# Performance work log

Hardware: AMD Instinct MI355X
Metric: run time of the kernel (lower is better)

The kernel has to match this reference:

```python
import jax, jax.numpy as jnp
import numpy as np

B, LQ, LK, D, H, DK = 128, 32, 128, 1024, 16, 64


def setup_inputs() -> dict:
    key = jax.random.key(0)
    ks = jax.random.split(key, 10)
    Q_seq = jax.random.normal(ks[0], (B, LQ, D), dtype=jnp.float32)
    K_seq = jax.random.normal(ks[1], (B, LK, D), dtype=jnp.float32)
    V_seq = jax.random.normal(ks[2], (B, LK, D), dtype=jnp.float32)
    title_mask = (jax.random.uniform(ks[3], (B, LQ)) < 0.9).astype(jnp.float32)
    body_mask = (jax.random.uniform(ks[4], (B, LQ, LK)) < 0.9).astype(jnp.float32)
    s = 1.0 / np.sqrt(D)
    Wq = jax.random.uniform(ks[5], (H * DK, D), jnp.float32, -s, s)
    Wk = jax.random.uniform(ks[6], (H * DK, D), jnp.float32, -s, s)
    Wv = jax.random.uniform(ks[7], (H * DK, D), jnp.float32, -s, s)
    bq = jnp.zeros((H * DK,), jnp.float32)
    bk = jnp.zeros((H * DK,), jnp.float32)
    bv = jnp.zeros((H * DK,), jnp.float32)
    return {"Q_seq": Q_seq, "K_seq": K_seq, "V_seq": V_seq,
            "title_mask": title_mask, "body_mask": body_mask,
            "Wq": Wq, "bq": bq, "Wk": Wk, "bk": bk, "Wv": Wv, "bv": bv}


def reference(Q_seq, K_seq, V_seq, title_mask, body_mask, Wq, bq, Wk, bk, Wv, bv):
    b = Q_seq.shape[0]
    # concatenate title tokens onto keys/values: [B, LK+LQ, D]
    K_cat = jnp.concatenate([K_seq, Q_seq], axis=1)
    V_cat = jnp.concatenate([V_seq, Q_seq], axis=1)
    # mask: [B, LQ, LK+LQ]
    tmask_rep = jnp.broadcast_to(title_mask[:, None, :], (b, LQ, LQ))
    mask = jnp.concatenate([body_mask, tmask_rep], axis=2) * title_mask[:, :, None]
    # projections -> [B, H, len, DK]
    Qh = (Q_seq @ Wq.T + bq).reshape(b, LQ, H, DK).transpose(0, 2, 1, 3)
    Kh = (K_cat @ Wk.T + bk).reshape(b, LK + LQ, H, DK).transpose(0, 2, 1, 3)
    Vh = (V_cat @ Wv.T + bv).reshape(b, LK + LQ, H, DK).transpose(0, 2, 1, 3)
    # custom exp-based masked attention (non-softmax normalization)
    scores = jnp.einsum('bhqd,bhkd->bhqk', Qh, Kh) / np.sqrt(float(DK))
    scores = jnp.exp(scores) * mask[:, None, :, :]
    attn = scores / (jnp.sum(scores, axis=-1, keepdims=True) + 1e-8)
    ctx = jnp.einsum('bhqk,bhkd->bhqd', attn, Vh)
    return ctx.transpose(0, 2, 1, 3).reshape(b, LQ, H * DK)
```

## Files before the change

### kernel.cpp

```cpp
#include <hip/hip_runtime.h>

typedef _Float16 f16;
typedef _Float16 f16x2 __attribute__((ext_vector_type(2)));
typedef _Float16 f16x4 __attribute__((ext_vector_type(4)));
typedef _Float16 f16x8 __attribute__((ext_vector_type(8)));
typedef float f32x4v __attribute__((ext_vector_type(4)));

#define AS1 __attribute__((address_space(1)))
#define AS3 __attribute__((address_space(3)))

__device__ __forceinline__ void gload_lds16(const f16* g, f16* l) {
  __builtin_amdgcn_global_load_lds((const AS1 unsigned int*)g,
                                   (AS3 unsigned int*)l, 16, 0, 0);
}

__global__ __launch_bounds__(256) void prep_kernel(
    const float* __restrict__ Q_seq, const float* __restrict__ K_seq,
    const float* __restrict__ V_seq,
    const float* __restrict__ Wq, const float* __restrict__ Wk,
    const float* __restrict__ Wv,
    f16* __restrict__ Qb, f16* __restrict__ Kb, f16* __restrict__ Vb,
    f16* __restrict__ Wqb, f16* __restrict__ Wkb, f16* __restrict__ Wvb)
{
  const long long g = (long long)blockIdx.x * 256 + threadIdx.x;
  const float* s;
  f16* d;
  if (g < 524288) {
    s = Q_seq + g * 8; d = Qb + g * 8;
  } else if (g < 2621440) {
    long long e = (g - 524288) * 8; s = K_seq + e; d = Kb + e;
  } else if (g < 4718592) {
    long long e = (g - 2621440) * 8; s = V_seq + e; d = Vb + e;
  } else if (g < 4849664) {
    long long e = (g - 4718592) * 8; s = Wq + e; d = Wqb + e;
  } else if (g < 4980736) {
    long long e = (g - 4849664) * 8; s = Wk + e; d = Wkb + e;
  } else {
    long long e = (g - 4980736) * 8; s = Wv + e; d = Wvb + e;
  }
  float4 v0 = *(const float4*)s;
  float4 v1 = *(const float4*)(s + 4);
  f16x8 o;
  o[0] = (f16)v0.x; o[1] = (f16)v0.y; o[2] = (f16)v0.z; o[3] = (f16)v0.w;
  o[4] = (f16)v1.x; o[5] = (f16)v1.y; o[6] = (f16)v1.z; o[7] = (f16)v1.w;
  *(f16x8*)d = o;
}

__device__ __forceinline__ void gemm_tile_128(
    const f16* __restrict__ A, const f16* __restrict__ W,
    const float* __restrict__ bias, f16* __restrict__ C,
    int m0, int n0, int rowShift, int outStride, int rowOff,
    f16* sbuf)
{
  f16* As0 = sbuf;
  f16* Bs0 = sbuf + 8192;

  const int t = threadIdx.x;
  const int w = t >> 6, lane = t & 63;
  const int wr = w >> 1, wc = w & 1;
  const int sr = lane >> 2, sc = (lane & 3) * 8;

  const f16* gA0 = A + (long long)(m0 + w * 32 + sr) * 1024 + sc;
  const f16* gA1 = A + (long long)(m0 + w * 32 + 16 + sr) * 1024 + sc;
  const f16* gB0 = W + (long long)(n0 + w * 32 + sr) * 1024 + sc;
  const f16* gB1 = W + (long long)(n0 + w * 32 + 16 + sr) * 1024 + sc;
  f16* lA0 = As0 + (w * 32) * 32;
  f16* lA1 = As0 + (w * 32 + 16) * 32;
  f16* lB0 = Bs0 + (w * 32) * 32;
  f16* lB1 = Bs0 + (w * 32 + 16) * 32;

  f32x4v acc[4][4];
#pragma unroll
  for (int i = 0; i < 4; ++i)
#pragma unroll
    for (int j = 0; j < 4; ++j) acc[i][j] = (f32x4v){0.f, 0.f, 0.f, 0.f};

  const int fr = lane & 15;
  const int fk = (lane >> 4) * 8;
  const f16* pA = As0 + (wr * 64 + fr) * 32 + fk;
  const f16* pB = Bs0 + (wc * 64 + fr) * 32 + fk;

  for (int k0 = 0; k0 < 1024; k0 += 64) {
    gload_lds16(gA0 + k0, lA0);
    gload_lds16(gA1 + k0, lA1);
    gload_lds16(gA0 + k0 + 32, lA0 + 4096);
    gload_lds16(gA1 + k0 + 32, lA1 + 4096);
    gload_lds16(gB0 + k0, lB0);
    gload_lds16(gB1 + k0, lB1);
    gload_lds16(gB0 + k0 + 32, lB0 + 4096);
    gload_lds16(gB1 + k0 + 32, lB1 + 4096);
    __syncthreads();
#pragma unroll
    for (int kk = 0; kk < 2; ++kk) {
      f16x8 av[4], bv[4];
#pragma unroll
      for (int i = 0; i < 4; ++i)
        av[i] = *(const f16x8*)(pA + kk * 4096 + i * 16 * 32);
#pragma unroll
      for (int i = 0; i < 4; ++i)
        bv[i] = *(const f16x8*)(pB + kk * 4096 + i * 16 * 32);
#pragma unroll
      for (int i = 0; i < 4; ++i)
#pragma unroll
        for (int j = 0; j < 4; ++j)
          acc[i][j] = __builtin_amdgcn_mfma_f32_16x16x32_f16(av[i], bv[j],
                                                             acc[i][j], 0, 0, 0);
    }
    __syncthreads();
  }

  f16* Cs = sbuf;
  float bn[4];
#pragma unroll
  for (int j = 0; j < 4; ++j) bn[j] = bias[n0 + wc * 64 + j * 16 + fr];
  const int g4 = (lane >> 4) * 4;
#pragma unroll
  for (int i = 0; i < 4; ++i) {
#pragma unroll
    for (int j = 0; j < 4; ++j) {
#pragma unroll
      for (int v = 0; v < 4; ++v) {
        int row = wr * 64 + i * 16 + g4 + v;
        int col = wc * 64 + j * 16 + fr;
        Cs[row * 136 + (col ^ ((row & 12) << 2))] = (f16)(acc[i][j][v] + bn[j]);
      }
    }
  }
  __syncthreads();

  const int rowMask = (1 << rowShift) - 1;
  const int row = t >> 1, half = t & 1;
  const int rsw = (row & 12) << 2;
  const int arow = m0 + row;
  const int orow = (arow >> rowShift) * outStride + (arow & rowMask) + rowOff;
  f16* dst = C + (long long)orow * 1024 + n0 + half * 64;
  const f16* srcr = Cs + row * 136;
#pragma unroll
  for (int c = 0; c < 8; ++c)
    *(f16x8*)(dst + c * 8) = *(const f16x8*)(srcr + ((half * 64 + c * 8) ^ rsw));
}

__global__ __launch_bounds__(256) void gemm_kv2(
    const f16* __restrict__ Kb, const f16* __restrict__ Wkb,
    const float* __restrict__ bk, f16* __restrict__ Kh,
    const f16* __restrict__ Vb, const f16* __restrict__ Wvb,
    const float* __restrict__ bv, f16* __restrict__ Vh)
{
  __shared__ __align__(16) f16 sbuf[128 * 136];
  const int bid = blockIdx.x;
  const int v = (bid & 7) * 256 + (bid >> 3);
  const int z = v >> 10, rem = v & 1023;
  const int by = rem >> 3, bx = rem & 7;
  const f16* A = z ? Vb : Kb;
  const f16* W = z ? Wvb : Wkb;
  const float* bias = z ? bv : bk;
  f16* C = z ? Vh : Kh;
  gemm_tile_128(A, W, bias, C, by * 128, bx * 128, 7, 160, 0, sbuf);
}

__global__ __launch_bounds__(256) void gemm_q3(
    const f16* __restrict__ Qb,
    const f16* __restrict__ Wqb, const f16* __restrict__ Wkb,
    const f16* __restrict__ Wvb,
    const float* __restrict__ bq, const float* __restrict__ bk,
    const float* __restrict__ bv,
    f16* __restrict__ Qh, f16* __restrict__ Kh, f16* __restrict__ Vh)
{
  __shared__ __align__(16) f16 sbuf[128 * 136];
  const int bid = blockIdx.x;
  const int v = (bid & 7) * 96 + (bid >> 3);
  const int z = v >> 8, rem = v & 255;
  const int by = rem >> 3, bx = rem & 7;
  const f16* W = (z == 0) ? Wqb : (z == 1) ? Wkb : Wvb;
  const float* bias = (z == 0) ? bq : (z == 1) ? bk : bv;
  f16* C = (z == 0) ? Qh : (z == 1) ? Kh : Vh;
  const int outStride = (z == 0) ? 32 : 160;
  const int rowOff = (z == 0) ? 0 : 128;
  gemm_tile_128(Qb, W, bias, C, by * 128, bx * 128, 5, outStride, rowOff, sbuf);
}

__global__ __launch_bounds__(256) void attn_kernel(
    const f16* __restrict__ Qh, const f16* __restrict__ Kh,
    const f16* __restrict__ Vh,
    const float* __restrict__ title, const float* __restrict__ body,
    float* __restrict__ out)
{
  __shared__ __align__(16) f16 Qs[32 * 72];
  __shared__ __align__(16) f16 Ks[160 * 72];
  __shared__ __align__(16) f16 Vs[160 * 68];
  __shared__ float rs[4][32];
  __shared__ float invs[32];

  const int bh = blockIdx.x, b = bh >> 4, h = bh & 15;
  const int t = threadIdx.x, w = t >> 6, lane = t & 63;
  const int c = lane & 15, g = lane >> 4;

  const long long qbase = ((long long)(b * 32) << 10) + h * 64;
  const long long kbase = ((long long)(b * 160) << 10) + h * 64;

  {
    int row = t >> 3, ch = t & 7;
    *(f16x8*)(Qs + row * 72 + ch * 8) =
        *(const f16x8*)(Qh + qbase + (long long)row * 1024 + ch * 8);
  }
#pragma unroll
  for (int r = 0; r < 5; ++r) {
    int i = t + r * 256;
    int row = i >> 3, ch = i & 7;
    *(f16x8*)(Ks + row * 72 + ch * 8) =
        *(const f16x8*)(Kh + kbase + (long long)row * 1024 + ch * 8);
    f16x8 vv = *(const f16x8*)(Vh + kbase + (long long)row * 1024 + ch * 8);
    f16x4 vlo = __builtin_shufflevector(vv, vv, 0, 1, 2, 3);
    f16x4 vhi = __builtin_shufflevector(vv, vv, 4, 5, 6, 7);
    *(f16x4*)(Vs + row * 68 + ch * 8) = vlo;
    *(f16x4*)(Vs + row * 68 + ch * 8 + 4) = vhi;
  }
  __syncthreads();

  f16x8 qf[2][2];
#pragma unroll
  for (int qt = 0; qt < 2; ++qt)
#pragma unroll
    for (int s = 0; s < 2; ++s)
      qf[qt][s] = *(const f16x8*)(Qs + (qt * 16 + c) * 72 + s * 32 + g * 8);

  const int cnt = (w < 2) ? 3 : 2;
  const int tile0 = (w < 2) ? w * 3 : 6 + (w - 2) * 2;

  f16x4 pp[3][2];
  float rsum[2] = {0.f, 0.f};

#pragma unroll
  for (int i = 0; i < 3; ++i) {
    if (i < cnt) {
      const int kt = tile0 + i;
      f16x8 kf0 = *(const f16x8*)(Ks + (kt * 16 + c) * 72 + 0 + g * 8);
      f16x8 kf1 = *(const f16x8*)(Ks + (kt * 16 + c) * 72 + 32 + g * 8);
#pragma unroll
      for (int qt = 0; qt < 2; ++qt) {
        f32x4v s4 = (f32x4v){0.f, 0.f, 0.f, 0.f};
        s4 = __builtin_amdgcn_mfma_f32_16x16x32_f16(kf0, qf[qt][0], s4, 0, 0, 0);
        s4 = __builtin_amdgcn_mfma_f32_16x16x32_f16(kf1, qf[qt][1], s4, 0, 0, 0);
        float4 m4;
        if (kt < 8) {
          m4 = *(const float4*)(body +
                ((long long)(b * 32 + qt * 16 + c)) * 128 + kt * 16 + 4 * g);
        } else {
          m4 = *(const float4*)(title + b * 32 + (kt - 8) * 16 + 4 * g);
        }
        float e0 = __expf(s4[0] * 0.125f) * m4.x;
        float e1 = __expf(s4[1] * 0.125f) * m4.y;
        float e2 = __expf(s4[2] * 0.125f) * m4.z;
        float e3 = __expf(s4[3] * 0.125f) * m4.w;
        rsum[qt] += (e0 + e1) + (e2 + e3);
        f16x4 p4;
        p4.x = (f16)e0; p4.y = (f16)e1; p4.z = (f16)e2; p4.w = (f16)e3;
        pp[i][qt] = p4;
      }
    }
  }

#pragma unroll
  for (int qt = 0; qt < 2; ++qt) {
    rsum[qt] += __shfl_xor(rsum[qt], 16);
    rsum[qt] += __shfl_xor(rsum[qt], 32);
  }
  if (lane < 16) {
    rs[w][c] = rsum[0];
    rs[w][16 + c] = rsum[1];
  }
  __syncthreads();

  f16* Ps = Ks;
#pragma unroll
  for (int i = 0; i < 3; ++i) {
    if (i < cnt) {
      const int kt = tile0 + i;
#pragma unroll
      for (int qt = 0; qt < 2; ++qt)
        *(f16x4*)(Ps + (qt * 16 + c) * 168 + kt * 16 + 4 * g) = pp[i][qt];
    }
  }
  if (t < 32) {
    float ssum = rs[0][t] + rs[1][t] + rs[2][t] + rs[3][t];
    invs[t] = title[b * 32 + t] / (ssum + 1e-8f);
  }
  __syncthreads();

  f32x4v o[2] = {(f32x4v){0.f, 0.f, 0.f, 0.f}, (f32x4v){0.f, 0.f, 0.f, 0.f}};
#pragma unroll
  for (int s = 0; s < 5; ++s) {
    f16x8 vf;
#pragma unroll
    for (int j = 0; j < 8; ++j)
      vf[j] = Vs[(32 * s + 8 * g + j) * 68 + 16 * w + c];
#pragma unroll
    for (int qt = 0; qt < 2; ++qt) {
      f16x8 pf = *(const f16x8*)(Ps + (qt * 16 + c) * 168 + s * 32 + g * 8);
      o[qt] = __builtin_amdgcn_mfma_f32_16x16x32_f16(pf, vf, o[qt], 0, 0, 0);
    }
  }

#pragma unroll
  for (int qt = 0; qt < 2; ++qt) {
#pragma unroll
    for (int v = 0; v < 4; ++v) {
      int q = qt * 16 + 4 * g + v;
      out[((long long)(b * 32 + q) << 10) + h * 64 + 16 * w + c] =
          o[qt][v] * invs[q];
    }
  }
}

extern "C" void kernel_launch(void* const* d_in, const int* in_sizes, int n_in,
                              void* d_out, int out_size, void* d_ws, size_t ws_size,
                              hipStream_t stream) {
  const float* Q_seq = (const float*)d_in[0];
  const float* K_seq = (const float*)d_in[1];
  const float* V_seq = (const float*)d_in[2];
  const float* title = (const float*)d_in[3];
  const float* body  = (const float*)d_in[4];
  const float* Wq = (const float*)d_in[5];
  const float* bq = (const float*)d_in[6];
  const float* Wk = (const float*)d_in[7];
  const float* bk = (const float*)d_in[8];
  const float* Wv = (const float*)d_in[9];
  const float* bv = (const float*)d_in[10];
  float* out = (float*)d_out;

  f16* ws = (f16*)d_ws;
  f16* Qb  = ws;
  f16* Kb  = Qb + 4194304;
  f16* Vb  = Kb + 16777216;
  f16* Wqb = Vb + 16777216;
  f16* Wkb = Wqb + 1048576;
  f16* Wvb = Wkb + 1048576;
  f16* Qh  = Wvb + 1048576;
  f16* Kh  = Qh + 4194304;
  f16* Vh  = Kh + 20971520;

  prep_kernel<<<19968, 256, 0, stream>>>(Q_seq, K_seq, V_seq, Wq, Wk, Wv,
                                         Qb, Kb, Vb, Wqb, Wkb, Wvb);
  gemm_kv2<<<2048, 256, 0, stream>>>(Kb, Wkb, bk, Kh, Vb, Wvb, bv, Vh);
  gemm_q3<<<768, 256, 0, stream>>>(Qb, Wqb, Wkb, Wvb, bq, bk, bv,
                                   Qh, Kh, Vh);
  attn_kernel<<<2048, 256, 0, stream>>>(Qh, Kh, Vh, title, body, out);
}
```

Baseline: 208.6 us.

## Enlarge projection GEMM tiles to 256x256 with double-buffered LDS pipeline

Replaces the 128x128 single-buffered GEMM tile with a 256x256 tile computed by 512 threads. The LDS buffers are double-buffered, with global_load_lds prefetch two K-tiles ahead, an XOR swizzle on the LDS layout, explicit waitcnt and barrier scheduling, and setprio around the MFMA bursts. The larger tile is meant to raise operand reuse and hide global-load latency behind MFMA work. In exchange it uses 128KB of LDS and occupancy of 1 block per CU, and gemm_q3 now launches only 192 blocks, which may underfill the GPU.

```diff
diff --git a/kernel.cpp b/kernel.cpp
--- a/kernel.cpp
+++ b/kernel.cpp
@@ -46,83 +46,119 @@
   *(f16x8*)d = o;
 }
 
-__device__ __forceinline__ void gemm_tile_128(
+__device__ __forceinline__ void gemm_tile_256(
     const f16* __restrict__ A, const f16* __restrict__ W,
     const float* __restrict__ bias, f16* __restrict__ C,
     int m0, int n0, int rowShift, int outStride, int rowOff,
     f16* sbuf)
 {
-  f16* As0 = sbuf;
-  f16* Bs0 = sbuf + 8192;
-
   const int t = threadIdx.x;
   const int w = t >> 6, lane = t & 63;
-  const int wr = w >> 1, wc = w & 1;
-  const int sr = lane >> 2, sc = (lane & 3) * 8;
-
-  const f16* gA0 = A + (long long)(m0 + w * 32 + sr) * 1024 + sc;
-  const f16* gA1 = A + (long long)(m0 + w * 32 + 16 + sr) * 1024 + sc;
-  const f16* gB0 = W + (long long)(n0 + w * 32 + sr) * 1024 + sc;
-  const f16* gB1 = W + (long long)(n0 + w * 32 + 16 + sr) * 1024 + sc;
-  f16* lA0 = As0 + (w * 32) * 32;
-  f16* lA1 = As0 + (w * 32 + 16) * 32;
-  f16* lB0 = Bs0 + (w * 32) * 32;
-  f16* lB1 = Bs0 + (w * 32 + 16) * 32;
-
-  f32x4v acc[4][4];
-#pragma unroll
-  for (int i = 0; i < 4; ++i)
+  const int wr = w >> 2, wc = w & 3;
+  const int fr = lane & 15, g = lane >> 4;
+  const int lrow = lane >> 3;
+  const int kgr = (lane & 7) ^ lrow;
+
+  const f16* aSrc[4];
+  const f16* bSrc[4];
+#pragma unroll
+  for (int s = 0; s < 4; ++s) {
+    aSrc[s] = A + (long long)(m0 + (w * 4 + s) * 8 + lrow) * 1024 + kgr * 8;
+    bSrc[s] = W + (long long)(n0 + (w * 4 + s) * 8 + lrow) * 1024 + kgr * 8;
+  }
+
+#define STAGE(tile)                                                          \
+  {                                                                          \
+    f16* ab_ = sbuf + (((tile) & 1) << 15);                                  \
+    const int ko_ = (tile) * 64;                                             \
+    _Pragma("unroll") for (int s = 0; s < 4; ++s)                            \
+        gload_lds16(aSrc[s] + ko_, ab_ + (w * 4 + s) * 512);                 \
+    _Pragma("unroll") for (int s = 0; s < 4; ++s)                            \
+        gload_lds16(bSrc[s] + ko_, ab_ + 16384 + (w * 4 + s) * 512);         \
+  }
+
+  const int gk0 = ((0 + g) ^ (fr & 7)) * 8;
+  const int gk1 = ((4 + g) ^ (fr & 7)) * 8;
+  const int aoff = (wr * 128 + fr) * 64;
+  const int boff = (wc * 64 + fr) * 64;
+
+  f32x4v acc[8][4];
+#pragma unroll
+  for (int i = 0; i < 8; ++i)
 #pragma unroll
     for (int j = 0; j < 4; ++j) acc[i][j] = (f32x4v){0.f, 0.f, 0.f, 0.f};
 
-  const int fr = lane & 15;
-  const int fk = (lane >> 4) * 8;
-  const f16* pA = As0 + (wr * 64 + fr) * 32 + fk;
-  const f16* pB = Bs0 + (wc * 64 + fr) * 32 + fk;
-
-  for (int k0 = 0; k0 < 1024; k0 += 64) {
-    gload_lds16(gA0 + k0, lA0);
-    gload_lds16(gA1 + k0, lA1);
-    gload_lds16(gA0 + k0 + 32, lA0 + 4096);
-    gload_lds16(gA1 + k0 + 32, lA1 + 4096);
-    gload_lds16(gB0 + k0, lB0);
-    gload_lds16(gB1 + k0, lB1);
-    gload_lds16(gB0 + k0 + 32, lB0 + 4096);
-    gload_lds16(gB1 + k0 + 32, lB1 + 4096);
-    __syncthreads();
-#pragma unroll
-    for (int kk = 0; kk < 2; ++kk) {
-      f16x8 av[4], bv[4];
-#pragma unroll
-      for (int i = 0; i < 4; ++i)
-        av[i] = *(const f16x8*)(pA + kk * 4096 + i * 16 * 32);
-#pragma unroll
-      for (int i = 0; i < 4; ++i)
-        bv[i] = *(const f16x8*)(pB + kk * 4096 + i * 16 * 32);
-#pragma unroll
-      for (int i = 0; i < 4; ++i)
-#pragma unroll
-        for (int j = 0; j < 4; ++j)
-          acc[i][j] = __builtin_amdgcn_mfma_f32_16x16x32_f16(av[i], bv[j],
-                                                             acc[i][j], 0, 0, 0);
-    }
-    __syncthreads();
-  }
+  STAGE(0);
+  STAGE(1);
+
+  for (int tt = 0; tt < 16; ++tt) {
+    if (tt < 15) {
+      asm volatile("s_waitcnt vmcnt(8)" ::: "memory");
+    } else {
+      asm volatile("s_waitcnt vmcnt(0)" ::: "memory");
+    }
+    __builtin_amdgcn_s_barrier();
+    __builtin_amdgcn_sched_barrier(0);
+
+    const f16* ab = sbuf + ((tt & 1) << 15);
+    const f16* bb = ab + 16384;
+
+    f16x8 av0[8], bv0[4];
+#pragma unroll
+    for (int i = 0; i < 8; ++i)
+      av0[i] = *(const f16x8*)(ab + aoff + i * 1024 + gk0);
+#pragma unroll
+    for (int j = 0; j < 4; ++j)
+      bv0[j] = *(const f16x8*)(bb + boff + j * 1024 + gk0);
+    asm volatile("s_waitcnt lgkmcnt(0)" ::: "memory");
+    __builtin_amdgcn_sched_barrier(0);
+    __builtin_amdgcn_s_setprio(1);
+#pragma unroll
+    for (int i = 0; i < 8; ++i)
+#pragma unroll
+      for (int j = 0; j < 4; ++j)
+        acc[i][j] = __builtin_amdgcn_mfma_f32_16x16x32_f16(av0[i], bv0[j],
+                                                           acc[i][j], 0, 0, 0);
+    __builtin_amdgcn_s_setprio(0);
+
+    f16x8 av1[8], bv1[4];
+#pragma unroll
+    for (int i = 0; i < 8; ++i)
+      av1[i] = *(const f16x8*)(ab + aoff + i * 1024 + gk1);
+#pragma unroll
+    for (int j = 0; j < 4; ++j)
+      bv1[j] = *(const f16x8*)(bb + boff + j * 1024 + gk1);
+    asm volatile("s_waitcnt lgkmcnt(0)" ::: "memory");
+    __builtin_amdgcn_sched_barrier(0);
+    __builtin_amdgcn_s_barrier();
+    __builtin_amdgcn_sched_barrier(0);
+    if (tt < 14) STAGE(tt + 2);
+    __builtin_amdgcn_sched_barrier(0);
+    __builtin_amdgcn_s_setprio(1);
+#pragma unroll
+    for (int i = 0; i < 8; ++i)
+#pragma unroll
+      for (int j = 0; j < 4; ++j)
+        acc[i][j] = __builtin_amdgcn_mfma_f32_16x16x32_f16(av1[i], bv1[j],
+                                                           acc[i][j], 0, 0, 0);
+    __builtin_amdgcn_s_setprio(0);
+  }
+#undef STAGE
 
   f16* Cs = sbuf;
   float bn[4];
 #pragma unroll
   for (int j = 0; j < 4; ++j) bn[j] = bias[n0 + wc * 64 + j * 16 + fr];
-  const int g4 = (lane >> 4) * 4;
-#pragma unroll
-  for (int i = 0; i < 4; ++i) {
+#pragma unroll
+  for (int i = 0; i < 8; ++i) {
 #pragma unroll
     for (int j = 0; j < 4; ++j) {
 #pragma unroll
       for (int v = 0; v < 4; ++v) {
-        int row = wr * 64 + i * 16 + g4 + v;
+        int row = wr * 128 + i * 16 + g * 4 + v;
         int col = wc * 64 + j * 16 + fr;
-        Cs[row * 136 + (col ^ ((row & 12) << 2))] = (f16)(acc[i][j][v] + bn[j]);
+        Cs[row * 256 + (col ^ (((row >> 2) & 7) << 3))] =
+            (f16)(acc[i][j][v] + bn[j]);
       }
     }
   }
@@ -130,35 +166,35 @@
 
   const int rowMask = (1 << rowShift) - 1;
   const int row = t >> 1, half = t & 1;
-  const int rsw = (row & 12) << 2;
+  const int csw = ((row >> 2) & 7) << 3;
   const int arow = m0 + row;
   const int orow = (arow >> rowShift) * outStride + (arow & rowMask) + rowOff;
-  f16* dst = C + (long long)orow * 1024 + n0 + half * 64;
-  const f16* srcr = Cs + row * 136;
-#pragma unroll
-  for (int c = 0; c < 8; ++c)
-    *(f16x8*)(dst + c * 8) = *(const f16x8*)(srcr + ((half * 64 + c * 8) ^ rsw));
-}
-
-__global__ __launch_bounds__(256) void gemm_kv2(
+  f16* dst = C + (long long)orow * 1024 + n0 + half * 128;
+  const f16* srcr = Cs + row * 256;
+#pragma unroll
+  for (int c = 0; c < 16; ++c)
+    *(f16x8*)(dst + c * 8) = *(const f16x8*)(srcr + ((half * 128 + c * 8) ^ csw));
+}
+
+__global__ __launch_bounds__(512, 1) void gemm_kv2(
     const f16* __restrict__ Kb, const f16* __restrict__ Wkb,
     const float* __restrict__ bk, f16* __restrict__ Kh,
     const f16* __restrict__ Vb, const f16* __restrict__ Wvb,
     const float* __restrict__ bv, f16* __restrict__ Vh)
 {
-  __shared__ __align__(16) f16 sbuf[128 * 136];
+  __shared__ __align__(16) f16 sbuf[65536];
   const int bid = blockIdx.x;
-  const int v = (bid & 7) * 256 + (bid >> 3);
-  const int z = v >> 10, rem = v & 1023;
-  const int by = rem >> 3, bx = rem & 7;
+  const int v = (bid & 7) * 64 + (bid >> 3);
+  const int z = v >> 8, rem = v & 255;
+  const int by = rem >> 2, bx = rem & 3;
   const f16* A = z ? Vb : Kb;
   const f16* W = z ? Wvb : Wkb;
   const float* bias = z ? bv : bk;
   f16* C = z ? Vh : Kh;
-  gemm_tile_128(A, W, bias, C, by * 128, bx * 128, 7, 160, 0, sbuf);
-}
-
-__global__ __launch_bounds__(256) void gemm_q3(
+  gemm_tile_256(A, W, bias, C, by * 256, bx * 256, 7, 160, 0, sbuf);
+}
+
+__global__ __launch_bounds__(512, 1) void gemm_q3(
     const f16* __restrict__ Qb,
     const f16* __restrict__ Wqb, const f16* __restrict__ Wkb,
     const f16* __restrict__ Wvb,
@@ -166,17 +202,17 @@
     const float* __restrict__ bv,
     f16* __restrict__ Qh, f16* __restrict__ Kh, f16* __restrict__ Vh)
 {
-  __shared__ __align__(16) f16 sbuf[128 * 136];
+  __shared__ __align__(16) f16 sbuf[65536];
   const int bid = blockIdx.x;
-  const int v = (bid & 7) * 96 + (bid >> 3);
-  const int z = v >> 8, rem = v & 255;
-  const int by = rem >> 3, bx = rem & 7;
+  const int v = (bid & 7) * 24 + (bid >> 3);
+  const int z = v >> 6, rem = v & 63;
+  const int by = rem >> 2, bx = rem & 3;
   const f16* W = (z == 0) ? Wqb : (z == 1) ? Wkb : Wvb;
   const float* bias = (z == 0) ? bq : (z == 1) ? bk : bv;
   f16* C = (z == 0) ? Qh : (z == 1) ? Kh : Vh;
   const int outStride = (z == 0) ? 32 : 160;
   const int rowOff = (z == 0) ? 0 : 128;
-  gemm_tile_128(Qb, W, bias, C, by * 128, bx * 128, 5, outStride, rowOff, sbuf);
+  gemm_tile_256(Qb, W, bias, C, by * 256, bx * 256, 5, outStride, rowOff, sbuf);
 }
 
 __global__ __launch_bounds__(256) void attn_kernel(
@@ -341,8 +377,8 @@
 
   prep_kernel<<<19968, 256, 0, stream>>>(Q_seq, K_seq, V_seq, Wq, Wk, Wv,
                                          Qb, Kb, Vb, Wqb, Wkb, Wvb);
-  gemm_kv2<<<2048, 256, 0, stream>>>(Kb, Wkb, bk, Kh, Vb, Wvb, bv, Vh);
-  gemm_q3<<<768, 256, 0, stream>>>(Qb, Wqb, Wkb, Wvb, bq, bk, bv,
+  gemm_kv2<<<512, 512, 0, stream>>>(Kb, Wkb, bk, Kh, Vb, Wvb, bv, Vh);
+  gemm_q3<<<192, 512, 0, stream>>>(Qb, Wqb, Wkb, Wvb, bq, bk, bv,
                                    Qh, Kh, Vh);
   attn_kernel<<<2048, 256, 0, stream>>>(Qh, Kh, Vh, title, body, out);
 }
```

After: 188.1 us. 9.8% less time.
